# Kernel tuning notes

Measured on AMD Instinct MI355X. Metric: run time of the kernel, lower is better.

## Reference

```python
import jax, jax.numpy as jnp
import numpy as np

B = 8
D = 512        # d_hidn
H = 8          # n_head
DH = 64        # d_head
L = 6          # n_layer
DFF = 2048     # d_ff
GRID = 10
DMLP = 1024
NOUT = 1
EPS = 1e-6
CIN = 2048
SEQ = 1 + 24 * 32 + 9 * 12 + 5 * 7  # 912


def setup_inputs() -> dict:
    key = jax.random.key(0)
    ks = jax.random.split(key, 40)
    rn = lambda k, s, sc=0.02: jax.random.normal(k, s, jnp.float32) * sc
    inp = {
        "feat_dis_org": jax.random.normal(ks[0], (B, CIN, 24, 32), jnp.float32),
        "feat_dis_ref_1": jax.random.normal(ks[1], (B, CIN, 9, 12), jnp.float32),
        "feat_dis_ref_2": jax.random.normal(ks[2], (B, CIN, 5, 7), jnp.float32),
        "conv_w": rn(ks[3], (D, CIN)),
        "conv_b": rn(ks[4], (D,)),
        "scale_org_emb": jax.random.uniform(ks[5], (D,), jnp.float32),
        "ref_1_emb": jax.random.uniform(ks[6], (D,), jnp.float32),
        "ref_2_emb": rn(ks[7], (D,), 1.0),
        "pos_emb": rn(ks[8], (GRID, GRID, D), 0.02),
        "cls_token": rn(ks[9], (D,), 0.02),
        "Wq": rn(ks[10], (L, D, D)), "bq": rn(ks[11], (L, D)),
        "Wk": rn(ks[12], (L, D, D)), "bk": rn(ks[13], (L, D)),
        "Wv": rn(ks[14], (L, D, D)), "bv": rn(ks[15], (L, D)),
        "Wo": rn(ks[16], (L, D, D)), "bo": rn(ks[17], (L, D)),
        "ln1_g": jnp.ones((L, D), jnp.float32), "ln1_b": jnp.zeros((L, D), jnp.float32),
        "w1": rn(ks[18], (L, DFF, D)), "b1": rn(ks[19], (L, DFF)),
        "w2": rn(ks[20], (L, D, DFF)), "b2": rn(ks[21], (L, D)),
        "ln2_g": jnp.ones((L, D), jnp.float32), "ln2_b": jnp.zeros((L, D), jnp.float32),
        "proj_w1": rn(ks[22], (DMLP, D)),
        "proj_w2": rn(ks[23], (NOUT, DMLP)),
        "mask_inputs": jnp.ones((B, SEQ), jnp.int32),
    }
    return inp


def _ln(x, g, b):
    m = jnp.mean(x, -1, keepdims=True)
    v = jnp.mean((x - m) ** 2, -1, keepdims=True)
    return (x - m) * jax.lax.rsqrt(v + EPS) * g + b


def _embed(feat, chan_emb, conv_w, conv_b, pos_emb):
    # 1x1 conv (conv_enc) as a channel contraction: [b,2048,h,w] -> [b,D,h,w]
    x = jnp.einsum('bchw,dc->bdhw', feat, conv_w) + conv_b[None, :, None, None]
    x = x + chan_emb[None, :, None, None]           # scale/ref embedding
    h, w = x.shape[2], x.shape[3]
    # vectorized version of the nested-loop gather: t_i = int(i/h*Grid)
    ti = (jnp.arange(h) * GRID) // h
    tj = (jnp.arange(w) * GRID) // w
    sp = pos_emb[ti][:, tj]                          # [h,w,D]
    x = x + jnp.transpose(sp, (2, 0, 1))[None]       # [b,D,h,w]
    return jnp.transpose(x.reshape(x.shape[0], D, h * w), (0, 2, 1))  # [b,hw,D]


def reference(feat_dis_org, feat_dis_ref_1, feat_dis_ref_2, conv_w, conv_b,
              scale_org_emb, ref_1_emb, ref_2_emb, pos_emb, cls_token,
              Wq, bq, Wk, bk, Wv, bv, Wo, bo, ln1_g, ln1_b,
              w1, b1, w2, b2, ln2_g, ln2_b, proj_w1, proj_w2, mask_inputs):
    t_org = _embed(feat_dis_org, scale_org_emb, conv_w, conv_b, pos_emb)
    t_r1 = _embed(feat_dis_ref_1, ref_1_emb, conv_w, conv_b, pos_emb)
    t_r2 = _embed(feat_dis_ref_2, ref_2_emb, conv_w, conv_b, pos_emb)
    cls = jnp.broadcast_to(cls_token[None, None, :], (B, 1, D))
    x = jnp.concatenate([cls, t_org, t_r1, t_r2], axis=1)   # [B,SEQ,D]

    pad = (mask_inputs == 0)[:, None, None, :]              # [B,1,1,SEQ]
    scale = 1.0 / (DH ** 0.5)

    for i in range(L):
        s = x.shape[1]
        q = (x @ Wq[i].T + bq[i]).reshape(B, s, H, DH).transpose(0, 2, 1, 3)
        k = (x @ Wk[i].T + bk[i]).reshape(B, s, H, DH).transpose(0, 2, 1, 3)
        v = (x @ Wv[i].T + bv[i]).reshape(B, s, H, DH).transpose(0, 2, 1, 3)
        scores = jnp.einsum('bhqd,bhkd->bhqk', q, k) * scale
        scores = jnp.where(pad, -1e9, scores)
        prob = jax.nn.softmax(scores, axis=-1)
        ctx = jnp.einsum('bhqk,bhkd->bhqd', prob, v)
        ctx = ctx.transpose(0, 2, 1, 3).reshape(B, s, H * DH)
        att = ctx @ Wo[i].T + bo[i]
        x = _ln(x + att, ln1_g[i], ln1_b[i])
        ff = jax.nn.gelu(x @ w1[i].T + b1[i], approximate=False) @ w2[i].T + b2[i]
        x = _ln(x + ff, ln2_g[i], ln2_b[i])

    cls_out = x[:, 0, :]
    hmlp = jax.nn.gelu(cls_out @ proj_w1.T, approximate=False)
    pred = hmlp @ proj_w2.T                                   # [B,1]
    return pred
```

## Files before the change

kernel.cpp:

```cpp
#include <hip/hip_runtime.h>
#include <hip/hip_bf16.h>
#include <math.h>

#define SEQ 912
#define NTOK 911
#define CIN_ 2048
#define NLAYER 6

typedef _Float16 f16x8 __attribute__((ext_vector_type(8)));
typedef _Float16 f16x4 __attribute__((ext_vector_type(4)));
typedef float f32x4 __attribute__((ext_vector_type(4)));

__device__ __forceinline__ float gelu_f(float x) {
    return 0.5f * x * (1.0f + erff(x * 0.70710678118654752f));
}

__device__ __forceinline__ int xcd_swizzle(int orig, int nwg) {
    int q = nwg >> 3, r = nwg & 7;
    int xcd = orig & 7, idx = orig >> 3;
    int base = (xcd < r) ? xcd * (q + 1) : r * (q + 1) + (xcd - r) * q;
    return base + idx;
}

__device__ __forceinline__ void gld16(const _Float16* g, _Float16* l) {
    __builtin_amdgcn_global_load_lds(
        (const __attribute__((address_space(1))) unsigned int*)g,
        (__attribute__((address_space(3))) unsigned int*)l,
        16, 0, 0);
}

__device__ __forceinline__ void stage_tile_g(const _Float16* Ab, const _Float16* Bb,
                                             size_t seg, _Float16* ldsW, int kk) {
    gld16(Ab + kk, ldsW);
    gld16(Ab + seg + kk, ldsW + 2048);
    gld16(Bb + kk, ldsW + 4096);
    gld16(Bb + seg + kk, ldsW + 6144);
}

__device__ __forceinline__ void compute_step_g(const _Float16* sb, int r0, int c0,
                                               int ln15, int quad, f32x4 (&acc)[4][4]) {
    f16x8 a[4], b[4];
#pragma unroll
    for (int i = 0; i < 4; ++i)
        a[i] = *(const f16x8*)&sb[(r0 + i * 16 + ln15) * 32 + quad * 8];
#pragma unroll
    for (int j = 0; j < 4; ++j)
        b[j] = *(const f16x8*)&sb[4096 + (c0 + j * 16 + ln15) * 32 + quad * 8];
#pragma unroll
    for (int i = 0; i < 4; ++i)
#pragma unroll
        for (int j = 0; j < 4; ++j)
            acc[i][j] = __builtin_amdgcn_mfma_f32_16x16x32_f16(a[i], b[j], acc[i][j], 0, 0, 0);
}

template <int ACT, int QKV>
__global__ __launch_bounds__(256) void gemm16(
    const _Float16* __restrict__ A, const _Float16* __restrict__ B,
    const float* __restrict__ bias, _Float16* __restrict__ Cout,
    _Float16* __restrict__ vT, int M, int N, int K, int ldc)
{
    __shared__ __align__(16) _Float16 smem[4 * 8192];
    _Float16* Cs = smem;
    const int t = threadIdx.x;
    const int nbx = N >> 7;
    const int swz = xcd_swizzle(blockIdx.x, gridDim.x);
    const int by = swz / nbx, bx = swz - by * nbx;
    const int m0 = by * 128, n0 = bx * 128;
    const int lane = t & 63, w = t >> 6;
    const int r0 = (w >> 1) * 64, c0 = (w & 1) * 64;
    const int ln15 = lane & 15, quad = lane >> 4;

    f32x4 zero = {0.f, 0.f, 0.f, 0.f};
    f32x4 acc[4][4];
#pragma unroll
    for (int i = 0; i < 4; ++i)
#pragma unroll
        for (int j = 0; j < 4; ++j) acc[i][j] = zero;

    const _Float16* Ab = A + (size_t)(m0 + w * 16 + (lane >> 2)) * K + (lane & 3) * 8;
    const _Float16* Bb = B + (size_t)(n0 + w * 16 + (lane >> 2)) * K + (lane & 3) * 8;
    const size_t seg = (size_t)64 * K;
    _Float16* ldsW = smem + w * 512;

    const int nK = K >> 5;
    stage_tile_g(Ab, Bb, seg, ldsW, 0);
    stage_tile_g(Ab, Bb, seg, ldsW + 8192, 32);

    for (int s = 0; s < nK - 2; ++s) {
        stage_tile_g(Ab, Bb, seg, ldsW + ((s + 2) & 3) * 8192, (s + 2) << 5);
        asm volatile("s_waitcnt vmcnt(8)" ::: "memory");
        __builtin_amdgcn_s_barrier();
        __builtin_amdgcn_sched_barrier(0);
        compute_step_g(smem + (s & 3) * 8192, r0, c0, ln15, quad, acc);
    }
    asm volatile("s_waitcnt vmcnt(4)" ::: "memory");
    __builtin_amdgcn_s_barrier();
    __builtin_amdgcn_sched_barrier(0);
    compute_step_g(smem + ((nK - 2) & 3) * 8192, r0, c0, ln15, quad, acc);
    asm volatile("s_waitcnt vmcnt(0)" ::: "memory");
    __builtin_amdgcn_s_barrier();
    __builtin_amdgcn_sched_barrier(0);
    compute_step_g(smem + ((nK - 1) & 3) * 8192, r0, c0, ln15, quad, acc);

    if (QKV && n0 >= 1024) {
#pragma unroll
        for (int j = 0; j < 4; ++j) {
            int gn = n0 + c0 + j * 16 + ln15;
            float bv = bias[gn];
            int chan = gn - 1024;
            int hh = chan >> 6, d = chan & 63;
#pragma unroll
            for (int i = 0; i < 4; ++i) {
                int gmBase = m0 + r0 + i * 16 + quad * 4;
                int bb = gmBase / 912, s = gmBase - bb * 912;
                f16x4 hv4;
#pragma unroll
                for (int r = 0; r < 4; ++r) hv4[r] = (_Float16)(acc[i][j][r] + bv);
                *(f16x4*)&vT[((size_t)((bb * 8 + hh) * 64 + d)) * 960 + s] = hv4;
            }
        }
    } else {
        __syncthreads();
#pragma unroll
        for (int half = 0; half < 2; ++half) {
            if ((w >> 1) == half) {
#pragma unroll
                for (int j = 0; j < 4; ++j) {
                    float bv = bias[n0 + c0 + j * 16 + ln15];
#pragma unroll
                    for (int i = 0; i < 4; ++i)
#pragma unroll
                        for (int r = 0; r < 4; ++r) {
                            float val = acc[i][j][r] + bv;
                            if (ACT == 1) val = gelu_f(val);
                            Cs[(i * 16 + quad * 4 + r) * 136 + c0 + j * 16 + ln15] = (_Float16)val;
                        }
                }
            }
            __syncthreads();
#pragma unroll
            for (int uu = 0; uu < 4; ++uu) {
                int u = t + uu * 256;
                int lr = u >> 4, ch = (u & 15) * 8;
                int gm = m0 + half * 64 + lr;
                if (gm < M)
                    *(f16x8*)&Cout[(size_t)gm * ldc + n0 + ch] = *(const f16x8*)&Cs[lr * 136 + ch];
            }
            __syncthreads();
        }
    }
}

__device__ __forceinline__ void stage_tile_s(const _Float16* Ab, const _Float16* Bb,
                                             size_t seg, _Float16* ldsW, int kk) {
    gld16(Ab + kk, ldsW);
    gld16(Ab + seg + kk, ldsW + 2048);
    gld16(Bb + kk, ldsW + 4096);
}

__device__ __forceinline__ void compute_step_s(const _Float16* sb, int r0, int c0,
                                               int ln15, int quad, f32x4 (&acc)[4][2]) {
    f16x8 a[4], b[2];
#pragma unroll
    for (int i = 0; i < 4; ++i)
        a[i] = *(const f16x8*)&sb[(r0 + i * 16 + ln15) * 32 + quad * 8];
#pragma unroll
    for (int j = 0; j < 2; ++j)
        b[j] = *(const f16x8*)&sb[4096 + (c0 + j * 16 + ln15) * 32 + quad * 8];
#pragma unroll
    for (int i = 0; i < 4; ++i)
#pragma unroll
        for (int j = 0; j < 2; ++j)
            acc[i][j] = __builtin_amdgcn_mfma_f32_16x16x32_f16(a[i], b[j], acc[i][j], 0, 0, 0);
}

__global__ __launch_bounds__(256) void gemm16_splitk(
    const _Float16* __restrict__ A, const _Float16* __restrict__ B,
    float* __restrict__ part, int M, int N, int K)
{
    __shared__ __align__(16) _Float16 smem[4 * 6144];
    const int t = threadIdx.x;
    const int nbx = N >> 6;
    const int swz = xcd_swizzle(blockIdx.x, gridDim.x);
    const int by = swz / nbx, bx = swz - by * nbx;
    const int m0 = by * 128, n0 = bx * 64;
    const int z = blockIdx.z;
    const int lane = t & 63, w = t >> 6;
    const int r0 = (w >> 1) * 64, c0 = (w & 1) * 32;
    const int ln15 = lane & 15, quad = lane >> 4;
    const int Ks = K >> 1;
    const int kBeg = z * Ks;

    f32x4 zero = {0.f, 0.f, 0.f, 0.f};
    f32x4 acc[4][2];
#pragma unroll
    for (int i = 0; i < 4; ++i)
#pragma unroll
        for (int j = 0; j < 2; ++j) acc[i][j] = zero;

    const _Float16* Ab = A + (size_t)(m0 + w * 16 + (lane >> 2)) * K + kBeg + (lane & 3) * 8;
    const _Float16* Bb = B + (size_t)(n0 + w * 16 + (lane >> 2)) * K + kBeg + (lane & 3) * 8;
    const size_t seg = (size_t)64 * K;
    _Float16* ldsW = smem + w * 512;

    const int nK = Ks >> 5;
    stage_tile_s(Ab, Bb, seg, ldsW, 0);
    stage_tile_s(Ab, Bb, seg, ldsW + 6144, 32);

    for (int s = 0; s < nK - 2; ++s) {
        stage_tile_s(Ab, Bb, seg, ldsW + ((s + 2) & 3) * 6144, (s + 2) << 5);
        asm volatile("s_waitcnt vmcnt(6)" ::: "memory");
        __builtin_amdgcn_s_barrier();
        __builtin_amdgcn_sched_barrier(0);
        compute_step_s(smem + (s & 3) * 6144, r0, c0, ln15, quad, acc);
    }
    asm volatile("s_waitcnt vmcnt(3)" ::: "memory");
    __builtin_amdgcn_s_barrier();
    __builtin_amdgcn_sched_barrier(0);
    compute_step_s(smem + ((nK - 2) & 3) * 6144, r0, c0, ln15, quad, acc);
    asm volatile("s_waitcnt vmcnt(0)" ::: "memory");
    __builtin_amdgcn_s_barrier();
    __builtin_amdgcn_sched_barrier(0);
    compute_step_s(smem + ((nK - 1) & 3) * 6144, r0, c0, ln15, quad, acc);

    float* out = part + (size_t)z * M * N;
#pragma unroll
    for (int j = 0; j < 2; ++j) {
        int gn = n0 + c0 + j * 16 + ln15;
#pragma unroll
        for (int i = 0; i < 4; ++i) {
            int gmBase = m0 + r0 + i * 16 + quad * 4;
#pragma unroll
            for (int r = 0; r < 4; ++r) {
                int gm = gmBase + r;
                if (gm < M) out[(size_t)gm * N + gn] = acc[i][j][r];
            }
        }
    }
}

__global__ __launch_bounds__(256) void cast16_kernel(
    const float* __restrict__ src, _Float16* __restrict__ dst, int n4)
{
    int i = blockIdx.x * 256 + threadIdx.x;
    if (i < n4) {
        float4 v = ((const float4*)src)[i];
        f16x4 h;
        h[0] = (_Float16)v.x; h[1] = (_Float16)v.y;
        h[2] = (_Float16)v.z; h[3] = (_Float16)v.w;
        ((f16x4*)dst)[i] = h;
    }
}

__global__ __launch_bounds__(256) void cast2_kernel(
    const float* __restrict__ s1, _Float16* __restrict__ d1, int n4_1,
    const float* __restrict__ s2, _Float16* __restrict__ d2, int n4_2)
{
    int i = blockIdx.x * 256 + threadIdx.x;
    if (i < n4_1) {
        float4 v = ((const float4*)s1)[i];
        f16x4 h;
        h[0] = (_Float16)v.x; h[1] = (_Float16)v.y;
        h[2] = (_Float16)v.z; h[3] = (_Float16)v.w;
        ((f16x4*)d1)[i] = h;
    } else {
        int j = i - n4_1;
        if (j < n4_2) {
            float4 v = ((const float4*)s2)[j];
            f16x4 h;
            h[0] = (_Float16)v.x; h[1] = (_Float16)v.y;
            h[2] = (_Float16)v.z; h[3] = (_Float16)v.w;
            ((f16x4*)d2)[j] = h;
        }
    }
}

__global__ __launch_bounds__(256) void pack_qkvw_kernel(
    const float* __restrict__ Wq, const float* __restrict__ Wk,
    const float* __restrict__ Wv, _Float16* __restrict__ dst)
{
    int idx = blockIdx.x * 256 + threadIdx.x;
    if (idx >= 6 * 1536 * 128) return;
    int c4 = idx & 127;
    int rc = idx >> 7;
    int r = rc % 1536;
    int l = rc / 1536;
    const float* src = (r < 512) ? Wq : (r < 1024) ? Wk : Wv;
    float4 v = *(const float4*)(src + ((size_t)l * 512 + (r & 511)) * 512 + c4 * 4);
    f16x4 h;
    h[0] = (_Float16)v.x; h[1] = (_Float16)v.y;
    h[2] = (_Float16)v.z; h[3] = (_Float16)v.w;
    *(f16x4*)(dst + ((size_t)l * 1536 + r) * 512 + c4 * 4) = h;
}

__global__ __launch_bounds__(256) void pack_qkvb_kernel(
    const float* __restrict__ bq, const float* __restrict__ bk,
    const float* __restrict__ bv, float* __restrict__ dst)
{
    int idx = blockIdx.x * 256 + threadIdx.x;
    if (idx < 6 * 1536) {
        int r = idx % 1536, l = idx / 1536;
        const float* s = (r < 512) ? bq : (r < 1024) ? bk : bv;
        dst[idx] = s[l * 512 + (r & 511)];
    }
}

__global__ __launch_bounds__(256) void transpose_feat_kernel(
    const float* __restrict__ feat, _Float16* __restrict__ patch, int HW, int tok_off)
{
    __shared__ float tile[32][33];
    const int b = blockIdx.z;
    const int c0 = blockIdx.y * 32;
    const int p0 = blockIdx.x * 32;
    const int tx = threadIdx.x, ty = threadIdx.y;
#pragma unroll
    for (int i = 0; i < 4; ++i) {
        int c = c0 + ty + i * 8;
        int p = p0 + tx;
        tile[ty + i * 8][tx] = (p < HW) ? feat[((size_t)b * CIN_ + c) * HW + p] : 0.f;
    }
    __syncthreads();
#pragma unroll
    for (int i = 0; i < 4; ++i) {
        int p = p0 + ty + i * 8;
        int c = c0 + tx;
        if (p < HW)
            patch[((size_t)(b * NTOK + tok_off + p)) * CIN_ + c] = (_Float16)tile[tx][ty + i * 8];
    }
}

__global__ __launch_bounds__(128) void build_x_red(
    const float* __restrict__ part, const float* __restrict__ conv_b,
    const float* __restrict__ cls_token,
    const float* __restrict__ emb_org, const float* __restrict__ emb_r1,
    const float* __restrict__ emb_r2, const float* __restrict__ pos_emb,
    float* __restrict__ x, _Float16* __restrict__ x16)
{
    const size_t ESTR = (size_t)7288 * 512;
    const int row = blockIdx.x;
    const int b = row / SEQ;
    const int tt = row - b * SEQ;
    const int d4 = threadIdx.x;
    float4 o;
    if (tt == 0) {
        o = ((const float4*)cls_token)[d4];
    } else {
        int tp = tt - 1;
        const float* ce; int hh, ww, p;
        if (tp < 768)      { p = tp;       hh = 24; ww = 32; ce = emb_org; }
        else if (tp < 876) { p = tp - 768; hh = 9;  ww = 12; ce = emb_r1; }
        else               { p = tp - 876; hh = 5;  ww = 7;  ce = emb_r2; }
        int i = p / ww, j = p - i * ww;
        int ti = (i * 10) / hh, tj = (j * 10) / ww;
        size_t prow = (size_t)(b * NTOK + tp) * 512;
        float4 t0 = ((const float4*)(part + prow))[d4];
        float4 t1 = ((const float4*)(part + ESTR + prow))[d4];
        float4 cb = ((const float4*)conv_b)[d4];
        float4 cv = ((const float4*)ce)[d4];
        float4 pv = ((const float4*)(pos_emb + (size_t)(ti * 10 + tj) * 512))[d4];
        o.x = t0.x + t1.x + cb.x + cv.x + pv.x;
        o.y = t0.y + t1.y + cb.y + cv.y + pv.y;
        o.z = t0.z + t1.z + cb.z + cv.z + pv.z;
        o.w = t0.w + t1.w + cb.w + cv.w + pv.w;
    }
    ((float4*)(x + (size_t)row * 512))[d4] = o;
    f16x4 h;
    h[0] = (_Float16)o.x; h[1] = (_Float16)o.y;
    h[2] = (_Float16)o.z; h[3] = (_Float16)o.w;
    ((f16x4*)(x16 + (size_t)row * 512))[d4] = h;
}

__global__ __launch_bounds__(64) void ln_residual_red(
    float* __restrict__ x, _Float16* __restrict__ x16,
    const float* __restrict__ part, const float* __restrict__ bias,
    const float* __restrict__ g, const float* __restrict__ bta)
{
    const size_t LSTR = (size_t)7296 * 512;
    const int row = blockIdx.x;
    const int t = threadIdx.x;
    float4* xr = (float4*)(x + (size_t)row * 512);
    const float4* p0 = (const float4*)(part + (size_t)row * 512);
    const float4* p1 = (const float4*)(part + LSTR + (size_t)row * 512);
    const float4* bb = (const float4*)bias;
    float4 a0 = xr[t], a1 = xr[t + 64];
    float4 q0 = p0[t], q1 = p0[t + 64];
    float4 r0 = p1[t], r1 = p1[t + 64];
    float4 c0 = bb[t], c1 = bb[t + 64];
    a0.x += q0.x + r0.x + c0.x; a0.y += q0.y + r0.y + c0.y;
    a0.z += q0.z + r0.z + c0.z; a0.w += q0.w + r0.w + c0.w;
    a1.x += q1.x + r1.x + c1.x; a1.y += q1.y + r1.y + c1.y;
    a1.z += q1.z + r1.z + c1.z; a1.w += q1.w + r1.w + c1.w;
    float s = a0.x + a0.y + a0.z + a0.w + a1.x + a1.y + a1.z + a1.w;
#pragma unroll
    for (int o = 32; o; o >>= 1) s += __shfl_xor(s, o, 64);
    const float mean = s * (1.f / 512.f);
    float sq = 0.f;
    sq += (a0.x - mean) * (a0.x - mean); sq += (a0.y - mean) * (a0.y - mean);
    sq += (a0.z - mean) * (a0.z - mean); sq += (a0.w - mean) * (a0.w - mean);
    sq += (a1.x - mean) * (a1.x - mean); sq += (a1.y - mean) * (a1.y - mean);
    sq += (a1.z - mean) * (a1.z - mean); sq += (a1.w - mean) * (a1.w - mean);
#pragma unroll
    for (int o = 32; o; o >>= 1) sq += __shfl_xor(sq, o, 64);
    const float rstd = rsqrtf(sq * (1.f / 512.f) + 1e-6f);
    const float4 g0 = ((const float4*)g)[t], g1 = ((const float4*)g)[t + 64];
    const float4 e0 = ((const float4*)bta)[t], e1 = ((const float4*)bta)[t + 64];
    float4 o0, o1;
    o0.x = (a0.x - mean) * rstd * g0.x + e0.x;
    o0.y = (a0.y - mean) * rstd * g0.y + e0.y;
    o0.z = (a0.z - mean) * rstd * g0.z + e0.z;
    o0.w = (a0.w - mean) * rstd * g0.w + e0.w;
    o1.x = (a1.x - mean) * rstd * g1.x + e1.x;
    o1.y = (a1.y - mean) * rstd * g1.y + e1.y;
    o1.z = (a1.z - mean) * rstd * g1.z + e1.z;
    o1.w = (a1.w - mean) * rstd * g1.w + e1.w;
    xr[t] = o0; xr[t + 64] = o1;
    f16x4 h0, h1;
    h0[0] = (_Float16)o0.x; h0[1] = (_Float16)o0.y;
    h0[2] = (_Float16)o0.z; h0[3] = (_Float16)o0.w;
    h1[0] = (_Float16)o1.x; h1[1] = (_Float16)o1.y;
    h1[2] = (_Float16)o1.z; h1[3] = (_Float16)o1.w;
    f16x4* xh = (f16x4*)(x16 + (size_t)row * 512);
    xh[t] = h0; xh[t + 64] = h1;
}

__global__ __launch_bounds__(256) void attn_mfma(
    const _Float16* __restrict__ qk, const _Float16* __restrict__ vT,
    const int* __restrict__ mask, _Float16* __restrict__ ctx)
{
    __shared__ __align__(16) _Float16 Ks[64 * 72];
    __shared__ __align__(16) _Float16 VTs[64 * 72];
    __shared__ __align__(16) _Float16 Pw[4][16 * 72];
    __shared__ float biasS[64];
    const int swz = xcd_swizzle(blockIdx.x, 960);
    const int qt = swz % 15;
    const int hb = swz / 15;
    const int h = hb & 7, b = hb >> 3;
    const int q0 = qt * 64;
    const int t = threadIdx.x;
    const int wave = t >> 6, lane = t & 63;
    const int ln15 = lane & 15, quad = lane >> 4;
    const int qrow = q0 + wave * 16 + ln15;

    f16x8 qf[2];
#pragma unroll
    for (int ks = 0; ks < 2; ++ks) {
        f16x8 z = {0, 0, 0, 0, 0, 0, 0, 0};
        qf[ks] = (qrow < SEQ)
            ? *(const f16x8*)(qk + (size_t)(b * SEQ + qrow) * 1024 + h * 64 + ks * 32 + quad * 8)
            : z;
    }

    f32x4 oacc[4];
    f32x4 zero = {0.f, 0.f, 0.f, 0.f};
#pragma unroll
    for (int dj = 0; dj < 4; ++dj) oacc[dj] = zero;
    float m_i = -1e30f, l_i = 0.f;

    for (int kb = 0; kb < 960; kb += 64) {
#pragma unroll
        for (int i = 0; i < 2; ++i) {
            int u = t + i * 256;
            int r = u >> 3, ch = (u & 7) * 8;
            int kg = kb + r;
            f16x8 kvv = {0, 0, 0, 0, 0, 0, 0, 0};
            if (kg < SEQ) kvv = *(const f16x8*)(qk + (size_t)(b * SEQ + kg) * 1024 + 512 + h * 64 + ch);
            *(f16x8*)&Ks[r * 72 + ch] = kvv;
            f16x8 vv = {0, 0, 0, 0, 0, 0, 0, 0};
            if (kb + ch < SEQ)
                vv = *(const f16x8*)(vT + ((size_t)((b * 8 + h) * 64 + r)) * 960 + kb + ch);
            *(f16x8*)&VTs[r * 72 + ch] = vv;
        }
        if (t < 64) {
            int kg = kb + t;
            biasS[t] = (kg < SEQ) ? (mask[b * SEQ + kg] ? 0.f : -1e9f) : -2e9f;
        }
        __syncthreads();

        f32x4 st[4];
#pragma unroll
        for (int jj = 0; jj < 4; ++jj) st[jj] = zero;
#pragma unroll
        for (int jj = 0; jj < 4; ++jj)
#pragma unroll
            for (int ks = 0; ks < 2; ++ks) {
                f16x8 kf = *(const f16x8*)&Ks[(jj * 16 + ln15) * 72 + ks * 32 + quad * 8];
                st[jj] = __builtin_amdgcn_mfma_f32_16x16x32_f16(kf, qf[ks], st[jj], 0, 0, 0);
            }

        float p[4][4];
        float mloc = -3e38f;
#pragma unroll
        for (int jj = 0; jj < 4; ++jj) {
            f32x4 bfr = *(const f32x4*)&biasS[jj * 16 + quad * 4];
#pragma unroll
            for (int r = 0; r < 4; ++r) {
                float sv = st[jj][r] * 0.125f + bfr[r];
                p[jj][r] = sv;
                mloc = fmaxf(mloc, sv);
            }
        }
        mloc = fmaxf(mloc, __shfl_xor(mloc, 16, 64));
        mloc = fmaxf(mloc, __shfl_xor(mloc, 32, 64));
        float mnew = fmaxf(m_i, mloc);
        float alpha = __expf(m_i - mnew);
        m_i = mnew;
        float sloc = 0.f;
#pragma unroll
        for (int jj = 0; jj < 4; ++jj)
#pragma unroll
            for (int r = 0; r < 4; ++r) {
                p[jj][r] = __expf(p[jj][r] - mnew);
                sloc += p[jj][r];
            }
        sloc += __shfl_xor(sloc, 16, 64);
        sloc += __shfl_xor(sloc, 32, 64);
        l_i = l_i * alpha + sloc;

        float ar[4];
#pragma unroll
        for (int r = 0; r < 4; ++r) ar[r] = __shfl(alpha, quad * 4 + r, 64);
#pragma unroll
        for (int dj = 0; dj < 4; ++dj)
#pragma unroll
            for (int r = 0; r < 4; ++r) oacc[dj][r] *= ar[r];

        _Float16* pw = &Pw[wave][0];
#pragma unroll
        for (int jj = 0; jj < 4; ++jj)
#pragma unroll
            for (int r = 0; r < 4; ++r)
                pw[ln15 * 72 + jj * 16 + quad * 4 + r] = (_Float16)p[jj][r];
        f16x8 pf[2];
#pragma unroll
        for (int ks = 0; ks < 2; ++ks)
            pf[ks] = *(const f16x8*)&pw[ln15 * 72 + ks * 32 + quad * 8];

#pragma unroll
        for (int dj = 0; dj < 4; ++dj)
#pragma unroll
            for (int ks = 0; ks < 2; ++ks) {
                f16x8 vf = *(const f16x8*)&VTs[(dj * 16 + ln15) * 72 + ks * 32 + quad * 8];
                oacc[dj] = __builtin_amdgcn_mfma_f32_16x16x32_f16(pf[ks], vf, oacc[dj], 0, 0, 0);
            }
        __syncthreads();
    }

    float linv[4];
#pragma unroll
    for (int r = 0; r < 4; ++r) linv[r] = 1.f / __shfl(l_i, quad * 4 + r, 64);
#pragma unroll
    for (int dj = 0; dj < 4; ++dj)
#pragma unroll
        for (int r = 0; r < 4; ++r) {
            int row = q0 + wave * 16 + quad * 4 + r;
            if (row < SEQ)
                ctx[(size_t)(b * SEQ + row) * 512 + h * 64 + dj * 16 + ln15] =
                    (_Float16)(oacc[dj][r] * linv[r]);
        }
}

__global__ __launch_bounds__(64) void head1_kernel(
    const float* __restrict__ x, const float* __restrict__ w,
    float* __restrict__ hmlp)
{
    const int n = blockIdx.x & 1023;
    const int b = blockIdx.x >> 10;
    const int t = threadIdx.x;
    const float4* cls = (const float4*)(x + (size_t)b * SEQ * 512);
    const float4* wr = (const float4*)(w + (size_t)n * 512);
    float s = 0.f;
#pragma unroll
    for (int i = 0; i < 2; ++i) {
        float4 a = cls[t + i * 64], c = wr[t + i * 64];
        s += a.x * c.x + a.y * c.y + a.z * c.z + a.w * c.w;
    }
#pragma unroll
    for (int o = 32; o; o >>= 1) s += __shfl_xor(s, o, 64);
    if (t == 0) hmlp[b * 1024 + n] = gelu_f(s);
}

__global__ __launch_bounds__(256) void head2_kernel(
    const float* __restrict__ hmlp, const float* __restrict__ w,
    float* __restrict__ out)
{
    __shared__ float red[4];
    const int b = blockIdx.x;
    const int t = threadIdx.x;
    float s = 0.f;
    for (int i = t; i < 1024; i += 256) s += hmlp[b * 1024 + i] * w[i];
#pragma unroll
    for (int o = 32; o; o >>= 1) s += __shfl_xor(s, o, 64);
    if ((t & 63) == 0) red[t >> 6] = s;
    __syncthreads();
    if (t == 0) out[b] = red[0] + red[1] + red[2] + red[3];
}

extern "C" void kernel_launch(void* const* d_in, const int* in_sizes, int n_in,
                              void* d_out, int out_size, void* d_ws, size_t ws_size,
                              hipStream_t stream)
{
    const float* feat_org = (const float*)d_in[0];
    const float* feat_r1  = (const float*)d_in[1];
    const float* feat_r2  = (const float*)d_in[2];
    const float* conv_w   = (const float*)d_in[3];
    const float* conv_b   = (const float*)d_in[4];
    const float* emb_org  = (const float*)d_in[5];
    const float* emb_r1   = (const float*)d_in[6];
    const float* emb_r2   = (const float*)d_in[7];
    const float* pos_emb  = (const float*)d_in[8];
    const float* cls_tok  = (const float*)d_in[9];
    const float* Wq = (const float*)d_in[10];
    const float* bq = (const float*)d_in[11];
    const float* Wk = (const float*)d_in[12];
    const float* bk = (const float*)d_in[13];
    const float* Wv = (const float*)d_in[14];
    const float* bv = (const float*)d_in[15];
    const float* Wo = (const float*)d_in[16];
    const float* bo = (const float*)d_in[17];
    const float* ln1g = (const float*)d_in[18];
    const float* ln1b = (const float*)d_in[19];
    const float* w1 = (const float*)d_in[20];
    const float* b1 = (const float*)d_in[21];
    const float* w2 = (const float*)d_in[22];
    const float* b2 = (const float*)d_in[23];
    const float* ln2g = (const float*)d_in[24];
    const float* ln2b = (const float*)d_in[25];
    const float* pw1 = (const float*)d_in[26];
    const float* pw2 = (const float*)d_in[27];
    const int*   mask = (const int*)d_in[28];

    char* base = (char*)d_ws;
    _Float16* ffh16 = (_Float16*)base;
    _Float16* patch16 = ffh16;
    base += (size_t)7296 * 2048 * 2;
    float* x = (float*)base; base += (size_t)7296 * 512 * 4;
    _Float16* qk16 = (_Float16*)base; base += (size_t)7296 * 1024 * 2;
    _Float16* vT16 = (_Float16*)base; base += (size_t)8 * 8 * 64 * 960 * 2;
    _Float16* ctx16 = (_Float16*)base; base += (size_t)7296 * 512 * 2;
    _Float16* x16   = (_Float16*)base; base += (size_t)7296 * 512 * 2;
    _Float16* wqkv_all = (_Float16*)base; base += (size_t)6 * 1536 * 512 * 2;
    _Float16* wo_all   = (_Float16*)base; base += (size_t)6 * 512 * 512 * 2;
    _Float16* w1_l16   = (_Float16*)base; base += (size_t)2048 * 512 * 2;
    _Float16* w2_l16   = (_Float16*)base; base += (size_t)512 * 2048 * 2;
    float* bqkv_all = (float*)base; base += 6 * 1536 * 4;
    float* hmlp = (float*)base; base += 8 * 1024 * 4;

    float* partO = (float*)ffh16;
    float* partF = (float*)qk16;
    _Float16* convw16 = x16;

    dim3 tb(32, 8);
    hipLaunchKernelGGL(transpose_feat_kernel, dim3(24, 64, 8), tb, 0, stream,
                       feat_org, patch16, 768, 0);
    hipLaunchKernelGGL(transpose_feat_kernel, dim3(4, 64, 8), tb, 0, stream,
                       feat_r1, patch16, 108, 768);
    hipLaunchKernelGGL(transpose_feat_kernel, dim3(2, 64, 8), tb, 0, stream,
                       feat_r2, patch16, 35, 876);
    hipLaunchKernelGGL(cast16_kernel, dim3(1024), 256, 0, stream,
                       conv_w, convw16, 512 * 2048 / 4);
    hipLaunchKernelGGL(cast16_kernel, dim3(1536), 256, 0, stream,
                       Wo, wo_all, 6 * 512 * 512 / 4);
    hipLaunchKernelGGL(pack_qkvw_kernel, dim3(4608), 256, 0, stream,
                       Wq, Wk, Wv, wqkv_all);
    hipLaunchKernelGGL(pack_qkvb_kernel, dim3(36), 256, 0, stream,
                       bq, bk, bv, bqkv_all);

    hipLaunchKernelGGL(gemm16_splitk, dim3(456, 1, 2), 256, 0, stream,
                       patch16, convw16, partF, 7288, 512, 2048);
    hipLaunchKernelGGL(build_x_red, dim3(7296), 128, 0, stream,
                       partF, conv_b, cls_tok, emb_org, emb_r1, emb_r2, pos_emb, x, x16);

    for (int l = 0; l < NLAYER; ++l) {
        hipLaunchKernelGGL(cast2_kernel, dim3(2048), 256, 0, stream,
                           w1 + (size_t)l * 2048 * 512, w1_l16, 2048 * 512 / 4,
                           w2 + (size_t)l * 512 * 2048, w2_l16, 512 * 2048 / 4);
        hipLaunchKernelGGL((gemm16<0, 1>), dim3(684), 256, 0, stream,
                           x16, wqkv_all + (size_t)l * 1536 * 512, bqkv_all + l * 1536,
                           qk16, vT16, 7296, 1536, 512, 1024);
        hipLaunchKernelGGL(attn_mfma, dim3(960), 256, 0, stream,
                           qk16, vT16, mask, ctx16);
        hipLaunchKernelGGL(gemm16_splitk, dim3(456, 1, 2), 256, 0, stream,
                           ctx16, wo_all + (size_t)l * 512 * 512, partO, 7296, 512, 512);
        hipLaunchKernelGGL(ln_residual_red, dim3(7296), 64, 0, stream,
                           x, x16, partO, bo + l * 512, ln1g + l * 512, ln1b + l * 512);
        hipLaunchKernelGGL((gemm16<1, 0>), dim3(912), 256, 0, stream,
                           x16, w1_l16, b1 + l * 2048,
                           ffh16, (_Float16*)nullptr, 7296, 2048, 512, 2048);
        hipLaunchKernelGGL(gemm16_splitk, dim3(456, 1, 2), 256, 0, stream,
                           ffh16, w2_l16, partF, 7296, 512, 2048);
        hipLaunchKernelGGL(ln_residual_red, dim3(7296), 64, 0, stream,
                           x, x16, partF, b2 + l * 512, ln2g + l * 512, ln2b + l * 512);
    }

    hipLaunchKernelGGL(head1_kernel, dim3(8 * 1024), 64, 0, stream, x, pw1, hmlp);
    hipLaunchKernelGGL(head2_kernel, dim3(8), 256, 0, stream, hmlp, pw2, (float*)d_out);
}
```

Baseline: 1.413 ms.

## Drop split-K for N=512 GEMMs and use triple-buffered LDS pipeline

Removes the two-way split-K from the conv, Wo and FFN2 GEMMs, so each block covers the full K and writes one fp32 output. The residual LayerNorm and embedding kernels then read a single partial buffer instead of summing two. Both GEMM kernels move from 4 LDS stages to 3, issuing the next tile's loads after the barrier instead of before it. This cuts partial-buffer traffic and LDS use, which may raise occupancy, but halves the grid for the N=512 GEMMs (456 blocks on 256 CUs) and prefetches one stage less deep.

```diff
diff --git a/kernel.cpp b/kernel.cpp
--- a/kernel.cpp
+++ b/kernel.cpp
@@ -59,7 +59,7 @@
     const float* __restrict__ bias, _Float16* __restrict__ Cout,
     _Float16* __restrict__ vT, int M, int N, int K, int ldc)
 {
-    __shared__ __align__(16) _Float16 smem[4 * 8192];
+    __shared__ __align__(16) _Float16 smem[3 * 8192];
     _Float16* Cs = smem;
     const int t = threadIdx.x;
     const int nbx = N >> 7;
@@ -87,20 +87,20 @@
     stage_tile_g(Ab, Bb, seg, ldsW + 8192, 32);
 
     for (int s = 0; s < nK - 2; ++s) {
-        stage_tile_g(Ab, Bb, seg, ldsW + ((s + 2) & 3) * 8192, (s + 2) << 5);
-        asm volatile("s_waitcnt vmcnt(8)" ::: "memory");
+        asm volatile("s_waitcnt vmcnt(4)" ::: "memory");
         __builtin_amdgcn_s_barrier();
         __builtin_amdgcn_sched_barrier(0);
-        compute_step_g(smem + (s & 3) * 8192, r0, c0, ln15, quad, acc);
+        stage_tile_g(Ab, Bb, seg, ldsW + ((s + 2) % 3) * 8192, (s + 2) << 5);
+        compute_step_g(smem + (s % 3) * 8192, r0, c0, ln15, quad, acc);
     }
     asm volatile("s_waitcnt vmcnt(4)" ::: "memory");
     __builtin_amdgcn_s_barrier();
     __builtin_amdgcn_sched_barrier(0);
-    compute_step_g(smem + ((nK - 2) & 3) * 8192, r0, c0, ln15, quad, acc);
+    compute_step_g(smem + ((nK - 2) % 3) * 8192, r0, c0, ln15, quad, acc);
     asm volatile("s_waitcnt vmcnt(0)" ::: "memory");
     __builtin_amdgcn_s_barrier();
     __builtin_amdgcn_sched_barrier(0);
-    compute_step_g(smem + ((nK - 1) & 3) * 8192, r0, c0, ln15, quad, acc);
+    compute_step_g(smem + ((nK - 1) % 3) * 8192, r0, c0, ln15, quad, acc);
 
     if (QKV && n0 >= 1024) {
 #pragma unroll
@@ -174,22 +174,19 @@
             acc[i][j] = __builtin_amdgcn_mfma_f32_16x16x32_f16(a[i], b[j], acc[i][j], 0, 0, 0);
 }
 
-__global__ __launch_bounds__(256) void gemm16_splitk(
+__global__ __launch_bounds__(256) void gemm16_p32(
     const _Float16* __restrict__ A, const _Float16* __restrict__ B,
-    float* __restrict__ part, int M, int N, int K)
-{
-    __shared__ __align__(16) _Float16 smem[4 * 6144];
+    float* __restrict__ out, int M, int N, int K)
+{
+    __shared__ __align__(16) _Float16 smem[3 * 6144];
     const int t = threadIdx.x;
     const int nbx = N >> 6;
     const int swz = xcd_swizzle(blockIdx.x, gridDim.x);
     const int by = swz / nbx, bx = swz - by * nbx;
     const int m0 = by * 128, n0 = bx * 64;
-    const int z = blockIdx.z;
     const int lane = t & 63, w = t >> 6;
     const int r0 = (w >> 1) * 64, c0 = (w & 1) * 32;
     const int ln15 = lane & 15, quad = lane >> 4;
-    const int Ks = K >> 1;
-    const int kBeg = z * Ks;
 
     f32x4 zero = {0.f, 0.f, 0.f, 0.f};
     f32x4 acc[4][2];
@@ -198,32 +195,31 @@
 #pragma unroll
         for (int j = 0; j < 2; ++j) acc[i][j] = zero;
 
-    const _Float16* Ab = A + (size_t)(m0 + w * 16 + (lane >> 2)) * K + kBeg + (lane & 3) * 8;
-    const _Float16* Bb = B + (size_t)(n0 + w * 16 + (lane >> 2)) * K + kBeg + (lane & 3) * 8;
+    const _Float16* Ab = A + (size_t)(m0 + w * 16 + (lane >> 2)) * K + (lane & 3) * 8;
+    const _Float16* Bb = B + (size_t)(n0 + w * 16 + (lane >> 2)) * K + (lane & 3) * 8;
     const size_t seg = (size_t)64 * K;
     _Float16* ldsW = smem + w * 512;
 
-    const int nK = Ks >> 5;
+    const int nK = K >> 5;
     stage_tile_s(Ab, Bb, seg, ldsW, 0);
     stage_tile_s(Ab, Bb, seg, ldsW + 6144, 32);
 
     for (int s = 0; s < nK - 2; ++s) {
-        stage_tile_s(Ab, Bb, seg, ldsW + ((s + 2) & 3) * 6144, (s + 2) << 5);
-        asm volatile("s_waitcnt vmcnt(6)" ::: "memory");
+        asm volatile("s_waitcnt vmcnt(3)" ::: "memory");
         __builtin_amdgcn_s_barrier();
         __builtin_amdgcn_sched_barrier(0);
-        compute_step_s(smem + (s & 3) * 6144, r0, c0, ln15, quad, acc);
+        stage_tile_s(Ab, Bb, seg, ldsW + ((s + 2) % 3) * 6144, (s + 2) << 5);
+        compute_step_s(smem + (s % 3) * 6144, r0, c0, ln15, quad, acc);
     }
     asm volatile("s_waitcnt vmcnt(3)" ::: "memory");
     __builtin_amdgcn_s_barrier();
     __builtin_amdgcn_sched_barrier(0);
-    compute_step_s(smem + ((nK - 2) & 3) * 6144, r0, c0, ln15, quad, acc);
+    compute_step_s(smem + ((nK - 2) % 3) * 6144, r0, c0, ln15, quad, acc);
     asm volatile("s_waitcnt vmcnt(0)" ::: "memory");
     __builtin_amdgcn_s_barrier();
     __builtin_amdgcn_sched_barrier(0);
-    compute_step_s(smem + ((nK - 1) & 3) * 6144, r0, c0, ln15, quad, acc);
-
-    float* out = part + (size_t)z * M * N;
+    compute_step_s(smem + ((nK - 1) % 3) * 6144, r0, c0, ln15, quad, acc);
+
 #pragma unroll
     for (int j = 0; j < 2; ++j) {
         int gn = n0 + c0 + j * 16 + ln15;
@@ -336,7 +332,6 @@
     const float* __restrict__ emb_r2, const float* __restrict__ pos_emb,
     float* __restrict__ x, _Float16* __restrict__ x16)
 {
-    const size_t ESTR = (size_t)7288 * 512;
     const int row = blockIdx.x;
     const int b = row / SEQ;
     const int tt = row - b * SEQ;
@@ -354,14 +349,13 @@
         int ti = (i * 10) / hh, tj = (j * 10) / ww;
         size_t prow = (size_t)(b * NTOK + tp) * 512;
         float4 t0 = ((const float4*)(part + prow))[d4];
-        float4 t1 = ((const float4*)(part + ESTR + prow))[d4];
         float4 cb = ((const float4*)conv_b)[d4];
         float4 cv = ((const float4*)ce)[d4];
         float4 pv = ((const float4*)(pos_emb + (size_t)(ti * 10 + tj) * 512))[d4];
-        o.x = t0.x + t1.x + cb.x + cv.x + pv.x;
-        o.y = t0.y + t1.y + cb.y + cv.y + pv.y;
-        o.z = t0.z + t1.z + cb.z + cv.z + pv.z;
-        o.w = t0.w + t1.w + cb.w + cv.w + pv.w;
+        o.x = t0.x + cb.x + cv.x + pv.x;
+        o.y = t0.y + cb.y + cv.y + pv.y;
+        o.z = t0.z + cb.z + cv.z + pv.z;
+        o.w = t0.w + cb.w + cv.w + pv.w;
     }
     ((float4*)(x + (size_t)row * 512))[d4] = o;
     f16x4 h;
@@ -375,21 +369,18 @@
     const float* __restrict__ part, const float* __restrict__ bias,
     const float* __restrict__ g, const float* __restrict__ bta)
 {
-    const size_t LSTR = (size_t)7296 * 512;
     const int row = blockIdx.x;
     const int t = threadIdx.x;
     float4* xr = (float4*)(x + (size_t)row * 512);
     const float4* p0 = (const float4*)(part + (size_t)row * 512);
-    const float4* p1 = (const float4*)(part + LSTR + (size_t)row * 512);
     const float4* bb = (const float4*)bias;
     float4 a0 = xr[t], a1 = xr[t + 64];
     float4 q0 = p0[t], q1 = p0[t + 64];
-    float4 r0 = p1[t], r1 = p1[t + 64];
     float4 c0 = bb[t], c1 = bb[t + 64];
-    a0.x += q0.x + r0.x + c0.x; a0.y += q0.y + r0.y + c0.y;
-    a0.z += q0.z + r0.z + c0.z; a0.w += q0.w + r0.w + c0.w;
-    a1.x += q1.x + r1.x + c1.x; a1.y += q1.y + r1.y + c1.y;
-    a1.z += q1.z + r1.z + c1.z; a1.w += q1.w + r1.w + c1.w;
+    a0.x += q0.x + c0.x; a0.y += q0.y + c0.y;
+    a0.z += q0.z + c0.z; a0.w += q0.w + c0.w;
+    a1.x += q1.x + c1.x; a1.y += q1.y + c1.y;
+    a1.z += q1.z + c1.z; a1.w += q1.w + c1.w;
     float s = a0.x + a0.y + a0.z + a0.w + a1.x + a1.y + a1.z + a1.w;
 #pragma unroll
     for (int o = 32; o; o >>= 1) s += __shfl_xor(s, o, 64);
@@ -665,7 +656,7 @@
     hipLaunchKernelGGL(pack_qkvb_kernel, dim3(36), 256, 0, stream,
                        bq, bk, bv, bqkv_all);
 
-    hipLaunchKernelGGL(gemm16_splitk, dim3(456, 1, 2), 256, 0, stream,
+    hipLaunchKernelGGL(gemm16_p32, dim3(456), 256, 0, stream,
                        patch16, convw16, partF, 7288, 512, 2048);
     hipLaunchKernelGGL(build_x_red, dim3(7296), 128, 0, stream,
                        partF, conv_b, cls_tok, emb_org, emb_r1, emb_r2, pos_emb, x, x16);
@@ -679,14 +670,14 @@
                            qk16, vT16, 7296, 1536, 512, 1024);
         hipLaunchKernelGGL(attn_mfma, dim3(960), 256, 0, stream,
                            qk16, vT16, mask, ctx16);
-        hipLaunchKernelGGL(gemm16_splitk, dim3(456, 1, 2), 256, 0, stream,
+        hipLaunchKernelGGL(gemm16_p32, dim3(456), 256, 0, stream,
                            ctx16, wo_all + (size_t)l * 512 * 512, partO, 7296, 512, 512);
         hipLaunchKernelGGL(ln_residual_red, dim3(7296), 64, 0, stream,
                            x, x16, partO, bo + l * 512, ln1g + l * 512, ln1b + l * 512);
         hipLaunchKernelGGL((gemm16<1, 0>), dim3(912), 256, 0, stream,
                            x16, w1_l16, b1 + l * 2048,
                            ffh16, (_Float16*)nullptr, 7296, 2048, 512, 2048);
-        hipLaunchKernelGGL(gemm16_splitk, dim3(456, 1, 2), 256, 0, stream,
+        hipLaunchKernelGGL(gemm16_p32, dim3(456), 256, 0, stream,
                            ffh16, w2_l16, partF, 7296, 512, 2048);
         hipLaunchKernelGGL(ln_residual_red, dim3(7296), 64, 0, stream,
                            x, x16, partF, b2 + l * 512, ln2g + l * 512, ln2b + l * 512);
```

After: 1.283 ms. -9.2%, faster.
